# Performance work log

Measured on AMD Instinct MI355X. Metric: run time of the kernel, lower is better.

Reference implementation:

```python
import jax, jax.numpy as jnp
import numpy as np

B, SX, SY, CIN, COUT, W, T = 16, 64, 64, 1, 1, 64, 20
YH = SY // 2 + 1  # rfft2 last-dim size


def _spec_conv(h, wr, wi):
    # h: [B, C, X, Y] real; w: [Cin, Cout, X, YH] complex (as real/imag pair)
    w = wr + 1j * wi
    hf = jnp.fft.rfft2(h, axes=(-2, -1))               # [B, Cin, X, YH]
    of = jnp.einsum('bixy,ioxy->boxy', hf, w)          # [B, Cout, X, YH]
    return jnp.fft.irfft2(of, s=(SX, SY), axes=(-2, -1))


def setup_inputs() -> dict:
    key = jax.random.key(0)
    ks = jax.random.split(key, 12)
    scale = 0.02
    x = jax.random.normal(ks[0], (B, SX, SY, CIN), dtype=jnp.float32)
    Wi = jax.random.normal(ks[1], (CIN, W), dtype=jnp.float32) * scale
    bi = jnp.zeros((W,), dtype=jnp.float32)
    Wo = jax.random.normal(ks[2], (W, COUT), dtype=jnp.float32) * scale
    bo = jnp.zeros((COUT,), dtype=jnp.float32)
    def spec(k):
        return jax.random.normal(k, (W, W, SX, YH), dtype=jnp.float32) * (1.0 / W)
    return {
        'x': x, 'num_time_steps': T,
        'Wi': Wi, 'bi': bi, 'Wo': Wo, 'bo': bo,
        'Wz_r': spec(ks[3]), 'Wz_i': spec(ks[4]),
        'Wr_r': spec(ks[5]), 'Wr_i': spec(ks[6]),
        'Wh_r': spec(ks[7]), 'Wh_i': spec(ks[8]),
    }


def reference(x, num_time_steps, Wi, bi, Wo, bo, Wz_r, Wz_i, Wr_r, Wr_i, Wh_r, Wh_i):
    h0 = x @ Wi + bi  # [B, X, Y, W]  (in_mapping)

    def step(h, _):
        hc = jnp.transpose(h, (0, 3, 1, 2))  # [B, W, X, Y]
        z = jax.nn.sigmoid(_spec_conv(hc, Wz_r, Wz_i))
        r = jax.nn.sigmoid(_spec_conv(hc, Wr_r, Wr_i))
        nh = jnp.tanh(_spec_conv(r * hc, Wh_r, Wh_i))
        hc = (1.0 - z) * hc + z * nh
        h = jnp.transpose(hc, (0, 2, 3, 1))  # back to [B, X, Y, W]
        y = h @ Wo + bo                      # out_mapping per step
        return h, y

    _, ys = jax.lax.scan(step, h0, xs=None, length=num_time_steps)
    # ys: [T, B, X, Y, COUT] -> [B, T, X, Y, COUT]
    return jnp.transpose(ys, (1, 0, 2, 3, 4))
```

## Files before the change

### kernel.cpp

```cpp
#include <hip/hip_runtime.h>
#include <math.h>


#define NIMG   1024
#define NFREQ  2112
#define IMGSZ  4096
#define INV_N  (1.0f/4096.0f)

constexpr int brev6(int i) {
    int r = 0;
    for (int b = 0; b < 6; ++b) r |= ((i >> b) & 1) << (5 - b);
    return r;
}

template <int DSIGN>
__device__ __forceinline__ void fft64(float* xr, float* xi,
                                      const float* cs, const float* sn) {
#pragma unroll
    for (int i = 0; i < 64; ++i) {
        const int j = brev6(i);
        if (j > i) {
            float tr = xr[i]; xr[i] = xr[j]; xr[j] = tr;
            float ti = xi[i]; xi[i] = xi[j]; xi[j] = ti;
        }
    }
#pragma unroll
    for (int s = 1; s <= 6; ++s) {
        const int m = 1 << s, h = m >> 1, step = 64 >> s;
#pragma unroll
        for (int j = 0; j < h; ++j) {
            const int tw = j * step;
            float c = 1.0f, sg = 0.0f;
            if (tw != 0) {
                c  = cs[tw];
                sg = (DSIGN < 0) ? -sn[tw] : sn[tw];
            }
#pragma unroll
            for (int k = j; k < 64; k += m) {
                const int p = k, q = k + h;
                const float vr = xr[q], vi = xi[q];
                float tr, ti;
                if (tw == 0) { tr = vr; ti = vi; }
                else         { tr = c * vr - sg * vi; ti = c * vi + sg * vr; }
                const float ur = xr[p], ui = xi[p];
                xr[p] = ur + tr; xi[p] = ui + ti;
                xr[q] = ur - tr; xi[q] = ui - ti;
            }
        }
    }
}

__device__ __forceinline__ void init_twiddles(float* cs, float* sn, int t) {
    float s, c;
    sincosf(6.28318530717958647692f * (float)t * (1.0f / 64.0f), &s, &c);
    cs[t] = c; sn[t] = s;
}

__device__ __forceinline__ float sigmoidf_(float v) {
    return 1.0f / (1.0f + expf(-v));
}

__device__ __forceinline__ void ifft_pass_x(const float2* __restrict__ F,
                                            float2* lds, const float* cs,
                                            const float* sn, int t) {
    __syncthreads();
    if (t < 33) {
        float ar[64], ai[64];
#pragma unroll
        for (int kx = 0; kx < 64; ++kx) {
            float2 v = F[kx * 33 + t];
            ar[kx] = v.x; ai[kx] = v.y;
        }
        fft64<1>(ar, ai, cs, sn);
#pragma unroll
        for (int x = 0; x < 64; ++x) lds[x * 33 + t] = make_float2(ar[x], ai[x]);
    }
    __syncthreads();
}

__device__ __forceinline__ void ifft_pass_y(const float2* lds, float* xr,
                                            float* xi, const float* cs,
                                            const float* sn, int t) {
#pragma unroll
    for (int k = 0; k <= 32; ++k) {
        float2 v = lds[t * 33 + k];
        xr[k] = v.x; xi[k] = v.y;
    }
#pragma unroll
    for (int k = 33; k < 64; ++k) {
        float2 v = lds[t * 33 + (64 - k)];
        xr[k] = v.x; xi[k] = -v.y;
    }
    fft64<1>(xr, xi, cs, sn);
}

__device__ __forceinline__ void fwd_pass_y(float* xr, float* xi, float2* lds,
                                           const float* cs, const float* sn,
                                           int t) {
    fft64<-1>(xr, xi, cs, sn);
#pragma unroll
    for (int k = 0; k <= 32; ++k) lds[t * 33 + k] = make_float2(xr[k], xi[k]);
}

__device__ __forceinline__ void fwd_pass_x(const float2* lds,
                                           float2* __restrict__ out,
                                           const float* cs, const float* sn,
                                           int t) {
    __syncthreads();
    if (t < 33) {
        float ar[64], ai[64];
#pragma unroll
        for (int x = 0; x < 64; ++x) {
            float2 v = lds[x * 33 + t];
            ar[x] = v.x; ai[x] = v.y;
        }
        fft64<-1>(ar, ai, cs, sn);
#pragma unroll
        for (int kx = 0; kx < 64; ++kx) out[kx * 33 + t] = make_float2(ar[kx], ai[kx]);
    }
}

__global__ __launch_bounds__(64) void k_h0fft(const float* __restrict__ x,
                                              const float* __restrict__ Wi,
                                              const float* __restrict__ bi,
                                              float* __restrict__ h,
                                              float2* __restrict__ Hf) {
    __shared__ float cs[64], sn[64];
    __shared__ float2 lds[64 * 33];
    const int t = threadIdx.x;
    init_twiddles(cs, sn, t);
    __syncthreads();
    const int ib = blockIdx.x;
    const int c = ib & 63, b = ib >> 6;
    const float wi = Wi[c], bc = bi[c];

    float xr[64], xi[64];
    const float4* xrow = (const float4*)(x + (size_t)b * IMGSZ + t * 64);
    float4* hrow = (float4*)(h + (size_t)ib * IMGSZ + t * 64);
#pragma unroll
    for (int k = 0; k < 16; ++k) {
        float4 v = xrow[k];
        v.x = v.x * wi + bc; v.y = v.y * wi + bc;
        v.z = v.z * wi + bc; v.w = v.w * wi + bc;
        hrow[k] = v;
        xr[4 * k + 0] = v.x; xr[4 * k + 1] = v.y;
        xr[4 * k + 2] = v.z; xr[4 * k + 3] = v.w;
    }
#pragma unroll
    for (int k = 0; k < 64; ++k) xi[k] = 0.0f;
    fwd_pass_y(xr, xi, lds, cs, sn, t);
    fwd_pass_x(lds, Hf + (size_t)ib * NFREQ, cs, sn, t);
}

__global__ __launch_bounds__(64) void k_fifft_r(const float2* __restrict__ Rf,
                                                const float* __restrict__ h,
                                                float2* __restrict__ RHf) {
    __shared__ float cs[64], sn[64];
    __shared__ float2 lds[64 * 33];
    const int t = threadIdx.x;
    init_twiddles(cs, sn, t);
    const size_t ib = blockIdx.x;
    float xr[64], xi[64];

    ifft_pass_x(Rf + ib * NFREQ, lds, cs, sn, t);
    ifft_pass_y(lds, xr, xi, cs, sn, t);
    const float4* h4 = (const float4*)(h + ib * IMGSZ + t * 64);
#pragma unroll
    for (int k = 0; k < 16; ++k) {
        float4 hv = h4[k];
        xr[4 * k + 0] = sigmoidf_(xr[4 * k + 0] * INV_N) * hv.x;
        xr[4 * k + 1] = sigmoidf_(xr[4 * k + 1] * INV_N) * hv.y;
        xr[4 * k + 2] = sigmoidf_(xr[4 * k + 2] * INV_N) * hv.z;
        xr[4 * k + 3] = sigmoidf_(xr[4 * k + 3] * INV_N) * hv.w;
    }
#pragma unroll
    for (int k = 0; k < 64; ++k) xi[k] = 0.0f;
    fwd_pass_y(xr, xi, lds, cs, sn, t);
    fwd_pass_x(lds, RHf + ib * NFREQ, cs, sn, t);
}

__global__ __launch_bounds__(64) void k_fifft_n(const float2* __restrict__ Nf,
                                                const float2* __restrict__ Zf,
                                                float* __restrict__ h,
                                                float2* __restrict__ Hfn) {
    __shared__ float cs[64], sn[64];
    __shared__ float2 lds[64 * 33];
    __shared__ float zbuf[64 * 64];
    const int t = threadIdx.x;
    init_twiddles(cs, sn, t);
    const size_t ib = blockIdx.x;
    float xr[64], xi[64];

    ifft_pass_x(Zf + ib * NFREQ, lds, cs, sn, t);
    ifft_pass_y(lds, xr, xi, cs, sn, t);
#pragma unroll
    for (int k = 0; k < 64; ++k) zbuf[t * 64 + k] = sigmoidf_(xr[k] * INV_N);

    ifft_pass_x(Nf + ib * NFREQ, lds, cs, sn, t);
    ifft_pass_y(lds, xr, xi, cs, sn, t);
    float4* h4 = (float4*)(h + ib * IMGSZ + t * 64);
    const float4* z4 = (const float4*)(zbuf + t * 64);
#pragma unroll
    for (int k = 0; k < 16; ++k) {
        float4 hv = h4[k];
        float4 zv = z4[k];
        hv.x = (1.0f - zv.x) * hv.x + zv.x * tanhf(xr[4 * k + 0] * INV_N);
        hv.y = (1.0f - zv.y) * hv.y + zv.y * tanhf(xr[4 * k + 1] * INV_N);
        hv.z = (1.0f - zv.z) * hv.z + zv.z * tanhf(xr[4 * k + 2] * INV_N);
        hv.w = (1.0f - zv.w) * hv.w + zv.w * tanhf(xr[4 * k + 3] * INV_N);
        h4[k] = hv;
        xr[4 * k + 0] = hv.x; xr[4 * k + 1] = hv.y;
        xr[4 * k + 2] = hv.z; xr[4 * k + 3] = hv.w;
    }
#pragma unroll
    for (int k = 0; k < 64; ++k) xi[k] = 0.0f;
    fwd_pass_y(xr, xi, lds, cs, sn, t);
    fwd_pass_x(lds, Hfn + ib * NFREQ, cs, sn, t);
}

__device__ __forceinline__ void cmadd4(float (&are)[4], float (&aim)[4],
                                       const float4 hA, const float4 hB,
                                       const float4 wr, const float4 wi) {
    are[0] += hA.x * wr.x - hA.y * wi.x;  aim[0] += hA.x * wi.x + hA.y * wr.x;
    are[1] += hA.z * wr.y - hA.w * wi.y;  aim[1] += hA.z * wi.y + hA.w * wr.y;
    are[2] += hB.x * wr.z - hB.y * wi.z;  aim[2] += hB.x * wi.z + hB.y * wr.z;
    are[3] += hB.z * wr.w - hB.w * wi.w;  aim[3] += hB.z * wi.w + hB.w * wr.w;
}

__global__ __launch_bounds__(256) void k_pw2(const float2* __restrict__ Hf,
                                             const float* __restrict__ wzr,
                                             const float* __restrict__ wzi,
                                             const float* __restrict__ wrr,
                                             const float* __restrict__ wri,
                                             float2* __restrict__ Zf,
                                             float2* __restrict__ Rf) {
    __shared__ float4 Wl[2][2][4][64];
    __shared__ float4 Hl[2][2][8][16];
    const int t  = threadIdx.x;
    const int l  = t & 63, w = t >> 6;
    const int fq = t & 7,  og = (t >> 3) & 7;
    const int o  = blockIdx.y * 8 + og;
    const int b0 = blockIdx.z * 8 + w * 2;
    const int fA = blockIdx.x * 32 + fq * 4;
    const size_t wstep = (size_t)64 * NFREQ;

    const int o_l = l >> 3, fq_l = l & 7;
    const float* wa = (w == 0) ? wzr : (w == 1) ? wzi : (w == 2) ? wrr : wri;
    const float* wsrc = wa + (size_t)(blockIdx.y * 8 + o_l) * NFREQ
                           + blockIdx.x * 32 + fq_l * 4;
    const int ski = w >> 1;
    const int sb  = (w & 1) * 4 + (l >> 4);
    const float2* hsrc = Hf + (size_t)((blockIdx.z * 8 + sb) * 64) * NFREQ
                            + blockIdx.x * 32 + (l & 15) * 2;

    float4 aw0, aw1, ah;
    float4 bw0, bw1, bh;

#define LOADB(ii, r0, r1, rh_) do {                                            \
        r0  = *(const float4*)(wsrc + (size_t)(2 * (ii)) * wstep);             \
        r1  = *(const float4*)(wsrc + (size_t)(2 * (ii) + 1) * wstep);         \
        rh_ = *(const float4*)(hsrc + (size_t)(2 * (ii) + ski) * NFREQ);       \
    } while (0)
#define WRITEB(bf, r0, r1, rh_) do {                                           \
        Wl[bf][0][w][l] = r0;                                                  \
        Wl[bf][1][w][l] = r1;                                                  \
        (&Hl[bf][ski][0][0])[(w & 1) * 64 + l] = rh_;                          \
    } while (0)
#define COMP(bf) do {                                                          \
        _Pragma("unroll")                                                      \
        for (int ki = 0; ki < 2; ++ki) {                                       \
            const float4 vzr = Wl[bf][ki][0][og * 8 + fq];                     \
            const float4 vzi = Wl[bf][ki][1][og * 8 + fq];                     \
            const float4 vrr = Wl[bf][ki][2][og * 8 + fq];                     \
            const float4 vri = Wl[bf][ki][3][og * 8 + fq];                     \
            _Pragma("unroll")                                                  \
            for (int bb = 0; bb < 2; ++bb) {                                   \
                const float4 hA = Hl[bf][ki][w * 2 + bb][2 * fq];              \
                const float4 hB = Hl[bf][ki][w * 2 + bb][2 * fq + 1];          \
                cmadd4(zre[bb], zim[bb], hA, hB, vzr, vzi);                    \
                cmadd4(rre[bb], rim[bb], hA, hB, vrr, vri);                    \
            }                                                                  \
        }                                                                      \
    } while (0)

    float zre[2][4], zim[2][4], rre[2][4], rim[2][4];
#pragma unroll
    for (int b = 0; b < 2; ++b)
#pragma unroll
        for (int k = 0; k < 4; ++k) {
            zre[b][k] = 0.0f; zim[b][k] = 0.0f;
            rre[b][k] = 0.0f; rim[b][k] = 0.0f;
        }

    LOADB(0, aw0, aw1, ah);
    WRITEB(0, aw0, aw1, ah);
    LOADB(1, bw0, bw1, bh);
    __syncthreads();

    for (int s = 0; s < 32; s += 2) {
        WRITEB(1, bw0, bw1, bh);
        if (s < 30) LOADB(s + 2, aw0, aw1, ah);
        COMP(0);
        __syncthreads();
        if (s < 30) WRITEB(0, aw0, aw1, ah);
        if (s < 28) LOADB(s + 3, bw0, bw1, bh);
        COMP(1);
        __syncthreads();
    }
#undef LOADB
#undef WRITEB
#undef COMP

#pragma unroll
    for (int b = 0; b < 2; ++b) {
        float4* pz = (float4*)(Zf + (size_t)((b0 + b) * 64 + o) * NFREQ + fA);
        float4* pr = (float4*)(Rf + (size_t)((b0 + b) * 64 + o) * NFREQ + fA);
        pz[0] = make_float4(zre[b][0], zim[b][0], zre[b][1], zim[b][1]);
        pz[1] = make_float4(zre[b][2], zim[b][2], zre[b][3], zim[b][3]);
        pr[0] = make_float4(rre[b][0], rim[b][0], rre[b][1], rim[b][1]);
        pr[1] = make_float4(rre[b][2], rim[b][2], rre[b][3], rim[b][3]);
    }
}

__global__ __launch_bounds__(256) void k_pw1(const float2* __restrict__ Hf,
                                             const float* __restrict__ whr,
                                             const float* __restrict__ whi,
                                             float2* __restrict__ Of) {
    __shared__ float4 Wl[2][2][2][64];
    __shared__ float4 Hl[2][2][8][16];
    const int t  = threadIdx.x;
    const int l  = t & 63, w = t >> 6;
    const int fq = t & 7,  og = (t >> 3) & 7;
    const int o  = blockIdx.y * 8 + og;
    const int b0 = blockIdx.z * 8 + w * 2;
    const int fA = blockIdx.x * 32 + fq * 4;
    const size_t wstep = (size_t)64 * NFREQ;

    const int o_l = l >> 3, fq_l = l & 7;
    const int ski = w >> 1, warr = w & 1;
    const float* wa = warr ? whi : whr;
    const float* wsrc = wa + (size_t)(blockIdx.y * 8 + o_l) * NFREQ
                           + blockIdx.x * 32 + fq_l * 4;
    const int sb  = (w & 1) * 4 + (l >> 4);
    const float2* hsrc = Hf + (size_t)((blockIdx.z * 8 + sb) * 64) * NFREQ
                            + blockIdx.x * 32 + (l & 15) * 2;

    float4 aw, ah;
    float4 bw, bh;

#define LOADB(ii, r0, rh_) do {                                                \
        r0  = *(const float4*)(wsrc + (size_t)(2 * (ii) + ski) * wstep);       \
        rh_ = *(const float4*)(hsrc + (size_t)(2 * (ii) + ski) * NFREQ);       \
    } while (0)
#define WRITEB(bf, r0, rh_) do {                                               \
        Wl[bf][ski][warr][l] = r0;                                             \
        (&Hl[bf][ski][0][0])[(w & 1) * 64 + l] = rh_;                          \
    } while (0)
#define COMP(bf) do {                                                          \
        _Pragma("unroll")                                                      \
        for (int ki = 0; ki < 2; ++ki) {                                       \
            const float4 vr = Wl[bf][ki][0][og * 8 + fq];                      \
            const float4 vi = Wl[bf][ki][1][og * 8 + fq];                      \
            _Pragma("unroll")                                                  \
            for (int bb = 0; bb < 2; ++bb) {                                   \
                const float4 hA = Hl[bf][ki][w * 2 + bb][2 * fq];              \
                const float4 hB = Hl[bf][ki][w * 2 + bb][2 * fq + 1];          \
                cmadd4(cre[bb], cim[bb], hA, hB, vr, vi);                      \
            }                                                                  \
        }                                                                      \
    } while (0)

    float cre[2][4], cim[2][4];
#pragma unroll
    for (int b = 0; b < 2; ++b)
#pragma unroll
        for (int k = 0; k < 4; ++k) { cre[b][k] = 0.0f; cim[b][k] = 0.0f; }

    LOADB(0, aw, ah);
    WRITEB(0, aw, ah);
    LOADB(1, bw, bh);
    __syncthreads();

    for (int s = 0; s < 32; s += 2) {
        WRITEB(1, bw, bh);
        if (s < 30) LOADB(s + 2, aw, ah);
        COMP(0);
        __syncthreads();
        if (s < 30) WRITEB(0, aw, ah);
        if (s < 28) LOADB(s + 3, bw, bh);
        COMP(1);
        __syncthreads();
    }
#undef LOADB
#undef WRITEB
#undef COMP

#pragma unroll
    for (int b = 0; b < 2; ++b) {
        float4* po = (float4*)(Of + (size_t)((b0 + b) * 64 + o) * NFREQ + fA);
        po[0] = make_float4(cre[b][0], cim[b][0], cre[b][1], cim[b][1]);
        po[1] = make_float4(cre[b][2], cim[b][2], cre[b][3], cim[b][3]);
    }
}

__global__ __launch_bounds__(256) void k_yproj(const float* __restrict__ h,
                                               const float* __restrict__ Wo,
                                               const float* __restrict__ bo,
                                               float* __restrict__ out,
                                               int step) {
    __shared__ float wo[64];
    const int t = threadIdx.x;
    if (t < 64) wo[t] = Wo[t];
    __syncthreads();
    const int b = blockIdx.x >> 4, xg = blockIdx.x & 15;
    const int xx = xg * 4 + (t >> 6), y = t & 63;
    const float* hp = h + (size_t)b * 64 * IMGSZ + xx * 64 + y;
    float acc = bo[0];
#pragma unroll 8
    for (int c = 0; c < 64; ++c) acc += hp[(size_t)c * IMGSZ] * wo[c];
    out[((size_t)b * 20 + step) * IMGSZ + xx * 64 + y] = acc;
}

extern "C" void kernel_launch(void* const* d_in, const int* in_sizes, int n_in,
                              void* d_out, int out_size, void* d_ws, size_t ws_size,
                              hipStream_t stream) {
    const float* x    = (const float*)d_in[0];
    const float* Wi   = (const float*)d_in[2];
    const float* bi   = (const float*)d_in[3];
    const float* Wo   = (const float*)d_in[4];
    const float* bo   = (const float*)d_in[5];
    const float* Wz_r = (const float*)d_in[6];
    const float* Wz_i = (const float*)d_in[7];
    const float* Wr_r = (const float*)d_in[8];
    const float* Wr_i = (const float*)d_in[9];
    const float* Wh_r = (const float*)d_in[10];
    const float* Wh_i = (const float*)d_in[11];

    float* ws = (float*)d_ws;
    float* h = ws;
    float2* B0 = (float2*)(ws + 4194304);
    float2* B1 = B0 + 2162688;
    float2* B2 = B1 + 2162688;
    float* outp = (float*)d_out;

    k_h0fft<<<NIMG, 64, 0, stream>>>(x, Wi, bi, h, B0);

    for (int t = 0; t < 20; ++t) {
        k_pw2<<<dim3(66, 8, 2), 256, 0, stream>>>(B0, Wz_r, Wz_i, Wr_r, Wr_i,
                                                  B1, B2);
        k_fifft_r<<<NIMG, 64, 0, stream>>>(B2, h, B2);
        k_pw1<<<dim3(66, 8, 2), 256, 0, stream>>>(B2, Wh_r, Wh_i, B0);
        k_fifft_n<<<NIMG, 64, 0, stream>>>(B0, B1, h, B0);
        k_yproj<<<256, 256, 0, stream>>>(h, Wo, bo, outp, t);
    }
}
```

Before: 4.303 ms.

## Stage FFT spectra through LDS with coalesced copies, pad zbuf, deepen GEMM prefetch

```diff
diff --git a/kernel.cpp b/kernel.cpp
--- a/kernel.cpp
+++ b/kernel.cpp
@@ -60,15 +60,29 @@
     return 1.0f / (1.0f + expf(-v));
 }
 
+
+__device__ __forceinline__ void copy_g2l(float4* dst, const float4* src, int t) {
+#pragma unroll
+    for (int j = 0; j < 16; ++j) dst[j * 64 + t] = src[j * 64 + t];
+    if (t < 32) dst[1024 + t] = src[1024 + t];
+}
+__device__ __forceinline__ void copy_l2g(float4* dst, const float4* src, int t) {
+#pragma unroll
+    for (int j = 0; j < 16; ++j) dst[j * 64 + t] = src[j * 64 + t];
+    if (t < 32) dst[1024 + t] = src[1024 + t];
+}
+
 __device__ __forceinline__ void ifft_pass_x(const float2* __restrict__ F,
                                             float2* lds, const float* cs,
                                             const float* sn, int t) {
     __syncthreads();
+    copy_g2l((float4*)lds, (const float4*)F, t);
+    __syncthreads();
     if (t < 33) {
         float ar[64], ai[64];
 #pragma unroll
         for (int kx = 0; kx < 64; ++kx) {
-            float2 v = F[kx * 33 + t];
+            float2 v = lds[kx * 33 + t];
             ar[kx] = v.x; ai[kx] = v.y;
         }
         fft64<1>(ar, ai, cs, sn);
@@ -102,7 +116,7 @@
     for (int k = 0; k <= 32; ++k) lds[t * 33 + k] = make_float2(xr[k], xi[k]);
 }
 
-__device__ __forceinline__ void fwd_pass_x(const float2* lds,
+__device__ __forceinline__ void fwd_pass_x(float2* lds,
                                            float2* __restrict__ out,
                                            const float* cs, const float* sn,
                                            int t) {
@@ -116,8 +130,10 @@
         }
         fft64<-1>(ar, ai, cs, sn);
 #pragma unroll
-        for (int kx = 0; kx < 64; ++kx) out[kx * 33 + t] = make_float2(ar[kx], ai[kx]);
-    }
+        for (int kx = 0; kx < 64; ++kx) lds[kx * 33 + t] = make_float2(ar[kx], ai[kx]);
+    }
+    __syncthreads();
+    copy_l2g((float4*)out, (const float4*)lds, t);
 }
 
 __global__ __launch_bounds__(64) void k_h0fft(const float* __restrict__ x,
@@ -126,7 +142,8 @@
                                               float* __restrict__ h,
                                               float2* __restrict__ Hf) {
     __shared__ float cs[64], sn[64];
-    __shared__ float2 lds[64 * 33];
+    __shared__ float4 lds4[1056];
+    float2* lds = (float2*)lds4;
     const int t = threadIdx.x;
     init_twiddles(cs, sn, t);
     __syncthreads();
@@ -156,7 +173,8 @@
                                                 const float* __restrict__ h,
                                                 float2* __restrict__ RHf) {
     __shared__ float cs[64], sn[64];
-    __shared__ float2 lds[64 * 33];
+    __shared__ float4 lds4[1056];
+    float2* lds = (float2*)lds4;
     const int t = threadIdx.x;
     init_twiddles(cs, sn, t);
     const size_t ib = blockIdx.x;
@@ -184,8 +202,9 @@
                                                 float* __restrict__ h,
                                                 float2* __restrict__ Hfn) {
     __shared__ float cs[64], sn[64];
-    __shared__ float2 lds[64 * 33];
-    __shared__ float zbuf[64 * 64];
+    __shared__ float4 lds4[1056];
+    __shared__ float zbuf[64 * 65];
+    float2* lds = (float2*)lds4;
     const int t = threadIdx.x;
     init_twiddles(cs, sn, t);
     const size_t ib = blockIdx.x;
@@ -194,20 +213,21 @@
     ifft_pass_x(Zf + ib * NFREQ, lds, cs, sn, t);
     ifft_pass_y(lds, xr, xi, cs, sn, t);
 #pragma unroll
-    for (int k = 0; k < 64; ++k) zbuf[t * 64 + k] = sigmoidf_(xr[k] * INV_N);
+    for (int k = 0; k < 64; ++k) zbuf[t * 65 + k] = sigmoidf_(xr[k] * INV_N);
 
     ifft_pass_x(Nf + ib * NFREQ, lds, cs, sn, t);
     ifft_pass_y(lds, xr, xi, cs, sn, t);
     float4* h4 = (float4*)(h + ib * IMGSZ + t * 64);
-    const float4* z4 = (const float4*)(zbuf + t * 64);
+    const float* zrow = zbuf + t * 65;
 #pragma unroll
     for (int k = 0; k < 16; ++k) {
         float4 hv = h4[k];
-        float4 zv = z4[k];
-        hv.x = (1.0f - zv.x) * hv.x + zv.x * tanhf(xr[4 * k + 0] * INV_N);
-        hv.y = (1.0f - zv.y) * hv.y + zv.y * tanhf(xr[4 * k + 1] * INV_N);
-        hv.z = (1.0f - zv.z) * hv.z + zv.z * tanhf(xr[4 * k + 2] * INV_N);
-        hv.w = (1.0f - zv.w) * hv.w + zv.w * tanhf(xr[4 * k + 3] * INV_N);
+        const float z0 = zrow[4 * k + 0], z1 = zrow[4 * k + 1];
+        const float z2 = zrow[4 * k + 2], z3 = zrow[4 * k + 3];
+        hv.x = (1.0f - z0) * hv.x + z0 * tanhf(xr[4 * k + 0] * INV_N);
+        hv.y = (1.0f - z1) * hv.y + z1 * tanhf(xr[4 * k + 1] * INV_N);
+        hv.z = (1.0f - z2) * hv.z + z2 * tanhf(xr[4 * k + 2] * INV_N);
+        hv.w = (1.0f - z3) * hv.w + z3 * tanhf(xr[4 * k + 3] * INV_N);
         h4[k] = hv;
         xr[4 * k + 0] = hv.x; xr[4 * k + 1] = hv.y;
         xr[4 * k + 2] = hv.z; xr[4 * k + 3] = hv.w;
@@ -295,15 +315,16 @@
     LOADB(0, aw0, aw1, ah);
     WRITEB(0, aw0, aw1, ah);
     LOADB(1, bw0, bw1, bh);
+    LOADB(2, aw0, aw1, ah);
     __syncthreads();
 
     for (int s = 0; s < 32; s += 2) {
         WRITEB(1, bw0, bw1, bh);
-        if (s < 30) LOADB(s + 2, aw0, aw1, ah);
+        if (s < 29) LOADB(s + 3, bw0, bw1, bh);
         COMP(0);
         __syncthreads();
         if (s < 30) WRITEB(0, aw0, aw1, ah);
-        if (s < 28) LOADB(s + 3, bw0, bw1, bh);
+        if (s < 28) LOADB(s + 4, aw0, aw1, ah);
         COMP(1);
         __syncthreads();
     }
@@ -379,15 +400,16 @@
     LOADB(0, aw, ah);
     WRITEB(0, aw, ah);
     LOADB(1, bw, bh);
+    LOADB(2, aw, ah);
     __syncthreads();
 
     for (int s = 0; s < 32; s += 2) {
         WRITEB(1, bw, bh);
-        if (s < 30) LOADB(s + 2, aw, ah);
+        if (s < 29) LOADB(s + 3, bw, bh);
         COMP(0);
         __syncthreads();
         if (s < 30) WRITEB(0, aw, ah);
-        if (s < 28) LOADB(s + 3, bw, bh);
+        if (s < 28) LOADB(s + 4, aw, ah);
         COMP(1);
         __syncthreads();
     }
```

Measured after the change: 4.226 ms. Within noise of the previous version (-1.8%).
